# Kernel optimization log

Measured on AMD Instinct MI355X. Metric: run time of the kernel, lower is better.

The kernel has to match this reference:

```python
import jax, jax.numpy as jnp
import numpy as np


def setup_inputs() -> dict:
    key = jax.random.key(0)
    k1, k2 = jax.random.split(key)
    B, D, H, W = 16, 64, 64, 64
    K = 1024  # codebook_size
    x = jax.random.normal(k1, (B, D, H, W), dtype=jnp.float32)
    codebook = jax.random.normal(k2, (K, D), dtype=jnp.float32)
    return {"x": x, "codebook": codebook}


def reference(x, codebook):
    """VQ quantization: nearest-codebook lookup.

    x: (B, D, H, W) latent features; codebook: (K, D).
    Returns (quantized (B, D, H, W), indices (B, H, W)).
    """
    B, D, H, W = x.shape
    # (B, D, H, W) -> (B*H*W, D)
    flat = jnp.transpose(x, (0, 2, 3, 1)).reshape(-1, D)
    d2 = (
        jnp.sum(flat * flat, axis=-1, keepdims=True)
        - 2.0 * (flat @ codebook.T)
        + jnp.sum(codebook * codebook, axis=-1)
    )
    idx = jnp.argmin(d2, axis=-1)  # (N,)
    quantized = codebook[idx]  # (N, D) gather
    quantized = quantized.reshape(B, H, W, D).transpose(0, 3, 1, 2)
    return quantized, idx.reshape(B, H, W)
```

## Files before the change

### kernel.cpp

```cpp
#include <hip/hip_runtime.h>
#include <hip/hip_bf16.h>

#define D_ 64
#define HW_ 4096
#define K_ 1024
#define NPTS_ 65536
#define QOUT_ 4194304
#define DELTA 0.006f
#define INF_ 3.4e38f

typedef short bf16x8 __attribute__((ext_vector_type(8)));
typedef float f32x4 __attribute__((ext_vector_type(4)));

__global__ __launch_bounds__(256) void vq_pack(const float* __restrict__ cb,
                                               float* __restrict__ cnorm,
                                               short* __restrict__ P) {
    const int t = blockIdx.x * 256 + threadIdx.x;
    const int gch = t >> 6, l = t & 63;
    const int j  = gch * 16 + (l & 15);
    const int dg = l >> 4;
#pragma unroll
    for (int s = 0; s < 2; ++s) {
        const float* src = cb + j * D_ + s * 32 + dg * 8;
        short hb[8], lb[8];
#pragma unroll
        for (int i = 0; i < 8; ++i) {
            const float v = -2.f * src[i];
            __hip_bfloat16 h = __float2bfloat16(v);
            hb[i] = *(const short*)&h;
            const float r = v - __bfloat162float(h);
            __hip_bfloat16 lo = __float2bfloat16(r);
            lb[i] = *(const short*)&lo;
        }
        short* dh = P + ((size_t)(gch * 4 + s * 2 + 0) * 64 + l) * 8;
        short* dl = P + ((size_t)(gch * 4 + s * 2 + 1) * 64 + l) * 8;
#pragma unroll
        for (int i = 0; i < 8; ++i) { dh[i] = hb[i]; dl[i] = lb[i]; }
    }
    if (t < K_) {
        const float4* r = (const float4*)(cb + (size_t)t * D_);
        float s0 = 0.f, s1 = 0.f, s2 = 0.f, s3 = 0.f;
#pragma unroll
        for (int i = 0; i < 16; ++i) {
            float4 v = r[i];
            s0 = fmaf(v.x, v.x, s0); s1 = fmaf(v.y, v.y, s1);
            s2 = fmaf(v.z, v.z, s2); s3 = fmaf(v.w, v.w, s3);
        }
        cnorm[t] = (s0 + s1) + (s2 + s3);
    }
}

__global__ __launch_bounds__(256, 2) void vq_main(const float* __restrict__ x,
                                                  const float* __restrict__ cb,
                                                  const float* __restrict__ cnorm_g,
                                                  const short* __restrict__ P,
                                                  float* __restrict__ out) {
    __shared__ float tile[64 * 69];
    __shared__ int res_idx[128];
    __shared__ int flist[128];
    __shared__ int fcnt;

    const int tid  = threadIdx.x;
    const int lane = tid & 63;
    const int wid  = tid >> 6;
    const int pg   = blockIdx.x;
    const int bb   = pg >> 5;
    const int hw0  = (pg & 31) << 7;

    if (tid == 0) fcnt = 0;

    bf16x8 ah[2][2], al[2][2];
    {
        const float* xb = x + (size_t)bb * (D_ * HW_) + hw0;
#pragma unroll
        for (int t = 0; t < 2; ++t) {
            const int p_l = wid * 32 + t * 16 + (lane & 15);
#pragma unroll
            for (int s = 0; s < 2; ++s) {
                const int d0 = s * 32 + (lane >> 4) * 8;
#pragma unroll
                for (int i = 0; i < 8; ++i) {
                    const float v = xb[(size_t)(d0 + i) * HW_ + p_l];
                    __hip_bfloat16 h = __float2bfloat16(v);
                    ah[t][s][i] = *(const short*)&h;
                    const float r = v - __bfloat162float(h);
                    __hip_bfloat16 lo = __float2bfloat16(r);
                    al[t][s][i] = *(const short*)&lo;
                }
            }
        }
    }
    __syncthreads();

    float m1[8], m2[8];
    int   i1[8];
#pragma unroll
    for (int q = 0; q < 8; ++q) { m1[q] = INF_; m2[q] = INF_; i1[q] = 0; }

    const bf16x8* gp = (const bf16x8*)P;
#pragma unroll 8
    for (int g = 0; g < 64; ++g) {
        const int kc = g * 16 + (lane & 15);
        const float cn = cnorm_g[kc];
        bf16x8 bh0 = gp[(g * 4 + 0) * 64 + lane];
        bf16x8 bl0 = gp[(g * 4 + 1) * 64 + lane];
        bf16x8 bh1 = gp[(g * 4 + 2) * 64 + lane];
        bf16x8 bl1 = gp[(g * 4 + 3) * 64 + lane];
        f32x4 a0a = {0.f, 0.f, 0.f, 0.f};
        f32x4 a0b = {0.f, 0.f, 0.f, 0.f};
        f32x4 a1a = {0.f, 0.f, 0.f, 0.f};
        f32x4 a1b = {0.f, 0.f, 0.f, 0.f};
        a0a = __builtin_amdgcn_mfma_f32_16x16x32_bf16(ah[0][0], bh0, a0a, 0, 0, 0);
        a1a = __builtin_amdgcn_mfma_f32_16x16x32_bf16(ah[1][0], bh0, a1a, 0, 0, 0);
        a0b = __builtin_amdgcn_mfma_f32_16x16x32_bf16(ah[0][1], bh1, a0b, 0, 0, 0);
        a1b = __builtin_amdgcn_mfma_f32_16x16x32_bf16(ah[1][1], bh1, a1b, 0, 0, 0);
        a0a = __builtin_amdgcn_mfma_f32_16x16x32_bf16(al[0][0], bh0, a0a, 0, 0, 0);
        a1a = __builtin_amdgcn_mfma_f32_16x16x32_bf16(al[1][0], bh0, a1a, 0, 0, 0);
        a0b = __builtin_amdgcn_mfma_f32_16x16x32_bf16(al[0][1], bh1, a0b, 0, 0, 0);
        a1b = __builtin_amdgcn_mfma_f32_16x16x32_bf16(al[1][1], bh1, a1b, 0, 0, 0);
        a0a = __builtin_amdgcn_mfma_f32_16x16x32_bf16(ah[0][0], bl0, a0a, 0, 0, 0);
        a1a = __builtin_amdgcn_mfma_f32_16x16x32_bf16(ah[1][0], bl0, a1a, 0, 0, 0);
        a0b = __builtin_amdgcn_mfma_f32_16x16x32_bf16(ah[0][1], bl1, a0b, 0, 0, 0);
        a1b = __builtin_amdgcn_mfma_f32_16x16x32_bf16(ah[1][1], bl1, a1b, 0, 0, 0);
#pragma unroll
        for (int t = 0; t < 2; ++t)
#pragma unroll
            for (int r = 0; r < 4; ++r) {
                const int q = t * 4 + r;
                const float d2 = cn + ((t == 0) ? (a0a[r] + a0b[r])
                                                : (a1a[r] + a1b[r]));
                const bool lt = d2 < m1[q];
                m2[q] = fminf(m2[q], fmaxf(m1[q], d2));
                m1[q] = fminf(m1[q], d2);
                i1[q] = lt ? kc : i1[q];
            }
    }

#pragma unroll
    for (int q = 0; q < 8; ++q) {
        float a1 = m1[q], a2 = m2[q];
        int   ai = i1[q];
#pragma unroll
        for (int m = 1; m < 16; m <<= 1) {
            const float o1 = __shfl_xor(a1, m);
            const int   oi = __shfl_xor(ai, m);
            const float o2 = __shfl_xor(a2, m);
            const float nm2 = fminf(fminf(a2, o2), fmaxf(a1, o1));
            if (o1 < a1 || (o1 == a1 && oi < ai)) { a1 = o1; ai = oi; }
            a2 = nm2;
        }
        if ((lane & 15) == 0) {
            const int t = q >> 2, r = q & 3;
            const int pt = wid * 32 + t * 16 + 4 * (lane >> 4) + r;
            res_idx[pt] = ai;
            if (a2 - a1 <= DELTA) { const int p = atomicAdd(&fcnt, 1); flist[p] = pt; }
        }
    }
    __syncthreads();

    const int nf = fcnt;
    for (int i = wid; i < nf; i += 4) {
        const int pt = flist[i];
        const float* xr = x + (size_t)bb * (D_ * HW_) + hw0 + pt;
        float xv[D_];
#pragma unroll
        for (int d = 0; d < D_; ++d) xv[d] = xr[(size_t)d * HW_];
        float b1 = INF_; int bi = 0;
        for (int cc = 0; cc < 16; ++cc) {
            const int row = lane * 16 + cc;
            const float4* cr = (const float4*)(cb + (size_t)row * D_);
            float a0 = 0.f, a1 = 0.f, a2 = 0.f, a3 = 0.f;
#pragma unroll
            for (int g = 0; g < 16; ++g) {
                const float4 cf = cr[g];
                a0 = fmaf(xv[4 * g + 0], cf.x, a0);
                a1 = fmaf(xv[4 * g + 1], cf.y, a1);
                a2 = fmaf(xv[4 * g + 2], cf.z, a2);
                a3 = fmaf(xv[4 * g + 3], cf.w, a3);
            }
            const float dot = (a0 + a1) + (a2 + a3);
            const float d2 = fmaf(-2.f, dot, cnorm_g[row]);
            if (d2 < b1) { b1 = d2; bi = row; }
        }
#pragma unroll
        for (int m = 1; m < 64; m <<= 1) {
            const float o1 = __shfl_xor(b1, m);
            const int   oi = __shfl_xor(bi, m);
            if (o1 < b1 || (o1 == b1 && oi < bi)) { b1 = o1; bi = oi; }
        }
        if (lane == 0) res_idx[pt] = bi;
    }
    __syncthreads();

    if (tid < 128) out[(size_t)QOUT_ + pg * 128 + tid] = (float)res_idx[tid];

#pragma unroll
    for (int pass = 0; pass < 8; ++pass) {
        const int pt = pass * 16 + (tid >> 4);
        const int dq = tid & 15;
        const float4 v = *(const float4*)(cb + (size_t)res_idx[pt] * D_ + dq * 4);
        tile[(dq * 4 + 0) * 69 + pt] = v.x;
        tile[(dq * 4 + 1) * 69 + pt] = v.y;
        tile[(dq * 4 + 2) * 69 + pt] = v.z;
        tile[(dq * 4 + 3) * 69 + pt] = v.w;
    }
    __syncthreads();

    float* ob = out + (size_t)bb * (D_ * HW_) + hw0;
#pragma unroll
    for (int it = 0; it < 8; ++it) {
        const int e = it * 256 + tid;
        const int d = e >> 5;
        const int g = e & 31;
        const float4 q = *(const float4*)&tile[d * 69 + g * 4];
        *(float4*)(ob + (size_t)d * HW_ + g * 4) = q;
    }
}

extern "C" void kernel_launch(void* const* d_in, const int* in_sizes, int n_in,
                              void* d_out, int out_size, void* d_ws, size_t ws_size,
                              hipStream_t stream) {
    const float* x  = (const float*)d_in[0];
    const float* cb = (const float*)d_in[1];
    float* out   = (float*)d_out;
    float* cnorm = (float*)d_ws;
    short* P     = (short*)((char*)d_ws + 4096);

    vq_pack<<<16, 256, 0, stream>>>(cb, cnorm, P);
    vq_main<<<NPTS_ / 128, 256, 0, stream>>>(x, cb, cnorm, P, out);
}
```

Baseline: 75.00 us.

## Stage packed codebook through LDS with triple-buffered async global-to-LDS loads

The packed codebook fragments and codebook norms are now streamed into shared memory with direct global-to-LDS loads, using a three-buffer rotation. Each chunk is prefetched two iterations ahead, and waitcnt plus barrier calls replace the per-iteration global loads in the MFMA loop. The shared buffer is reused afterwards as the transpose tile, with a new 65-stride layout. The aim is to hide global load latency and cut redundant L2 traffic, since every wave used to reload the same fragments. The cost is more LDS per block, which may reduce occupancy, plus a barrier in every chunk.

Measured after the change: 62.15 us. 1.21x faster.

```diff
diff --git a/kernel.cpp b/kernel.cpp
--- a/kernel.cpp
+++ b/kernel.cpp
@@ -8,9 +8,19 @@
 #define QOUT_ 4194304
 #define DELTA 0.006f
 #define INF_ 3.4e38f
+#define NCH 16
 
 typedef short bf16x8 __attribute__((ext_vector_type(8)));
 typedef float f32x4 __attribute__((ext_vector_type(4)));
+
+__device__ __forceinline__ void gload_lds16(const float* g, float* l) {
+    __builtin_amdgcn_global_load_lds((const __attribute__((address_space(1))) void*)g,
+                                     (__attribute__((address_space(3))) void*)l, 16, 0, 0);
+}
+__device__ __forceinline__ void gload_lds4(const float* g, float* l) {
+    __builtin_amdgcn_global_load_lds((const __attribute__((address_space(1))) void*)g,
+                                     (__attribute__((address_space(3))) void*)l, 4, 0, 0);
+}
 
 __global__ __launch_bounds__(256) void vq_pack(const float* __restrict__ cb,
                                                float* __restrict__ cnorm,
@@ -50,12 +60,21 @@
     }
 }
 
+__device__ __forceinline__ void stage_chunk(const float* src, float* dst,
+                                            int wid, int lane) {
+#pragma unroll
+    for (int r = 0; r < 4; ++r)
+        gload_lds16(src + (wid * 4 + r) * 256 + lane * 4,
+                    dst + (wid * 4 + r) * 256);
+}
+
 __global__ __launch_bounds__(256, 2) void vq_main(const float* __restrict__ x,
                                                   const float* __restrict__ cb,
                                                   const float* __restrict__ cnorm_g,
                                                   const short* __restrict__ P,
                                                   float* __restrict__ out) {
-    __shared__ float tile[64 * 69];
+    __shared__ short cbuf[3][8192];
+    __shared__ float cnt[K_];
     __shared__ int res_idx[128];
     __shared__ int flist[128];
     __shared__ int fcnt;
@@ -68,6 +87,17 @@
     const int hw0  = (pg & 31) << 7;
 
     if (tid == 0) fcnt = 0;
+
+    const float* Pf = (const float*)P;
+    float* buf0 = (float*)cbuf[0];
+    float* buf1 = (float*)cbuf[1];
+    float* buf2 = (float*)cbuf[2];
+
+#pragma unroll
+    for (int r = 0; r < 4; ++r)
+        gload_lds4(cnorm_g + (wid * 4 + r) * 64 + lane, cnt + (wid * 4 + r) * 64);
+    stage_chunk(Pf, buf0, wid, lane);
+    stage_chunk(Pf + 4096, buf1, wid, lane);
 
     bf16x8 ah[2][2], al[2][2];
     {
@@ -90,50 +120,67 @@
             }
         }
     }
-    __syncthreads();
+    asm volatile("s_waitcnt vmcnt(4)" ::: "memory");
+    __builtin_amdgcn_s_barrier();
+    asm volatile("" ::: "memory");
 
     float m1[8], m2[8];
     int   i1[8];
 #pragma unroll
     for (int q = 0; q < 8; ++q) { m1[q] = INF_; m2[q] = INF_; i1[q] = 0; }
 
-    const bf16x8* gp = (const bf16x8*)P;
-#pragma unroll 8
-    for (int g = 0; g < 64; ++g) {
-        const int kc = g * 16 + (lane & 15);
-        const float cn = cnorm_g[kc];
-        bf16x8 bh0 = gp[(g * 4 + 0) * 64 + lane];
-        bf16x8 bl0 = gp[(g * 4 + 1) * 64 + lane];
-        bf16x8 bh1 = gp[(g * 4 + 2) * 64 + lane];
-        bf16x8 bl1 = gp[(g * 4 + 3) * 64 + lane];
-        f32x4 a0a = {0.f, 0.f, 0.f, 0.f};
-        f32x4 a0b = {0.f, 0.f, 0.f, 0.f};
-        f32x4 a1a = {0.f, 0.f, 0.f, 0.f};
-        f32x4 a1b = {0.f, 0.f, 0.f, 0.f};
-        a0a = __builtin_amdgcn_mfma_f32_16x16x32_bf16(ah[0][0], bh0, a0a, 0, 0, 0);
-        a1a = __builtin_amdgcn_mfma_f32_16x16x32_bf16(ah[1][0], bh0, a1a, 0, 0, 0);
-        a0b = __builtin_amdgcn_mfma_f32_16x16x32_bf16(ah[0][1], bh1, a0b, 0, 0, 0);
-        a1b = __builtin_amdgcn_mfma_f32_16x16x32_bf16(ah[1][1], bh1, a1b, 0, 0, 0);
-        a0a = __builtin_amdgcn_mfma_f32_16x16x32_bf16(al[0][0], bh0, a0a, 0, 0, 0);
-        a1a = __builtin_amdgcn_mfma_f32_16x16x32_bf16(al[1][0], bh0, a1a, 0, 0, 0);
-        a0b = __builtin_amdgcn_mfma_f32_16x16x32_bf16(al[0][1], bh1, a0b, 0, 0, 0);
-        a1b = __builtin_amdgcn_mfma_f32_16x16x32_bf16(al[1][1], bh1, a1b, 0, 0, 0);
-        a0a = __builtin_amdgcn_mfma_f32_16x16x32_bf16(ah[0][0], bl0, a0a, 0, 0, 0);
-        a1a = __builtin_amdgcn_mfma_f32_16x16x32_bf16(ah[1][0], bl0, a1a, 0, 0, 0);
-        a0b = __builtin_amdgcn_mfma_f32_16x16x32_bf16(ah[0][1], bl1, a0b, 0, 0, 0);
-        a1b = __builtin_amdgcn_mfma_f32_16x16x32_bf16(ah[1][1], bl1, a1b, 0, 0, 0);
-#pragma unroll
-        for (int t = 0; t < 2; ++t)
-#pragma unroll
-            for (int r = 0; r < 4; ++r) {
-                const int q = t * 4 + r;
-                const float d2 = cn + ((t == 0) ? (a0a[r] + a0b[r])
-                                                : (a1a[r] + a1b[r]));
-                const bool lt = d2 < m1[q];
-                m2[q] = fminf(m2[q], fmaxf(m1[q], d2));
-                m1[q] = fminf(m1[q], d2);
-                i1[q] = lt ? kc : i1[q];
-            }
+    float* bcur = buf0;
+    float* bnxt = buf1;
+    float* bstg = buf2;
+#pragma unroll 1
+    for (int c = 0; c < NCH; ++c) {
+        if (c + 2 < NCH) stage_chunk(Pf + (size_t)(c + 2) * 4096, bstg, wid, lane);
+
+        const bf16x8* fr = (const bf16x8*)bcur;
+#pragma unroll
+        for (int gl = 0; gl < 4; ++gl) {
+            const int kc = c * 64 + gl * 16 + (lane & 15);
+            const float cn = cnt[kc];
+            bf16x8 bh0 = fr[(gl * 4 + 0) * 64 + lane];
+            bf16x8 bl0 = fr[(gl * 4 + 1) * 64 + lane];
+            bf16x8 bh1 = fr[(gl * 4 + 2) * 64 + lane];
+            bf16x8 bl1 = fr[(gl * 4 + 3) * 64 + lane];
+            f32x4 a0a = {0.f, 0.f, 0.f, 0.f};
+            f32x4 a0b = {0.f, 0.f, 0.f, 0.f};
+            f32x4 a1a = {0.f, 0.f, 0.f, 0.f};
+            f32x4 a1b = {0.f, 0.f, 0.f, 0.f};
+            a0a = __builtin_amdgcn_mfma_f32_16x16x32_bf16(ah[0][0], bh0, a0a, 0, 0, 0);
+            a1a = __builtin_amdgcn_mfma_f32_16x16x32_bf16(ah[1][0], bh0, a1a, 0, 0, 0);
+            a0b = __builtin_amdgcn_mfma_f32_16x16x32_bf16(ah[0][1], bh1, a0b, 0, 0, 0);
+            a1b = __builtin_amdgcn_mfma_f32_16x16x32_bf16(ah[1][1], bh1, a1b, 0, 0, 0);
+            a0a = __builtin_amdgcn_mfma_f32_16x16x32_bf16(al[0][0], bh0, a0a, 0, 0, 0);
+            a1a = __builtin_amdgcn_mfma_f32_16x16x32_bf16(al[1][0], bh0, a1a, 0, 0, 0);
+            a0b = __builtin_amdgcn_mfma_f32_16x16x32_bf16(al[0][1], bh1, a0b, 0, 0, 0);
+            a1b = __builtin_amdgcn_mfma_f32_16x16x32_bf16(al[1][1], bh1, a1b, 0, 0, 0);
+            a0a = __builtin_amdgcn_mfma_f32_16x16x32_bf16(ah[0][0], bl0, a0a, 0, 0, 0);
+            a1a = __builtin_amdgcn_mfma_f32_16x16x32_bf16(ah[1][0], bl0, a1a, 0, 0, 0);
+            a0b = __builtin_amdgcn_mfma_f32_16x16x32_bf16(ah[0][1], bl1, a0b, 0, 0, 0);
+            a1b = __builtin_amdgcn_mfma_f32_16x16x32_bf16(ah[1][1], bl1, a1b, 0, 0, 0);
+#pragma unroll
+            for (int t = 0; t < 2; ++t)
+#pragma unroll
+                for (int r = 0; r < 4; ++r) {
+                    const int q = t * 4 + r;
+                    const float d2 = cn + ((t == 0) ? (a0a[r] + a0b[r])
+                                                    : (a1a[r] + a1b[r]));
+                    const bool lt = d2 < m1[q];
+                    m2[q] = fminf(m2[q], fmaxf(m1[q], d2));
+                    m1[q] = fminf(m1[q], d2);
+                    i1[q] = lt ? kc : i1[q];
+                }
+        }
+
+        if (c + 2 < NCH) asm volatile("s_waitcnt vmcnt(4)" ::: "memory");
+        else             asm volatile("s_waitcnt vmcnt(0)" ::: "memory");
+        __builtin_amdgcn_s_barrier();
+        asm volatile("" ::: "memory");
+
+        float* t0 = bcur; bcur = bnxt; bnxt = bstg; bstg = t0;
     }
 
 #pragma unroll
@@ -179,7 +226,7 @@
                 a3 = fmaf(xv[4 * g + 3], cf.w, a3);
             }
             const float dot = (a0 + a1) + (a2 + a3);
-            const float d2 = fmaf(-2.f, dot, cnorm_g[row]);
+            const float d2 = fmaf(-2.f, dot, cnt[row]);
             if (d2 < b1) { b1 = d2; bi = row; }
         }
 #pragma unroll
@@ -194,15 +241,16 @@
 
     if (tid < 128) out[(size_t)QOUT_ + pg * 128 + tid] = (float)res_idx[tid];
 
+    float* tile = (float*)cbuf;
 #pragma unroll
     for (int pass = 0; pass < 8; ++pass) {
         const int pt = pass * 16 + (tid >> 4);
         const int dq = tid & 15;
         const float4 v = *(const float4*)(cb + (size_t)res_idx[pt] * D_ + dq * 4);
-        tile[(dq * 4 + 0) * 69 + pt] = v.x;
-        tile[(dq * 4 + 1) * 69 + pt] = v.y;
-        tile[(dq * 4 + 2) * 69 + pt] = v.z;
-        tile[(dq * 4 + 3) * 69 + pt] = v.w;
+        tile[pt * 65 + dq * 4 + 0] = v.x;
+        tile[pt * 65 + dq * 4 + 1] = v.y;
+        tile[pt * 65 + dq * 4 + 2] = v.z;
+        tile[pt * 65 + dq * 4 + 3] = v.w;
     }
     __syncthreads();
 
@@ -212,7 +260,11 @@
         const int e = it * 256 + tid;
         const int d = e >> 5;
         const int g = e & 31;
-        const float4 q = *(const float4*)&tile[d * 69 + g * 4];
+        float4 q;
+        q.x = tile[(g * 4 + 0) * 65 + d];
+        q.y = tile[(g * 4 + 1) * 65 + d];
+        q.z = tile[(g * 4 + 2) * 65 + d];
+        q.w = tile[(g * 4 + 3) * 65 + d];
         *(float4*)(ob + (size_t)d * HW_ + g * 4) = q;
     }
 }
```
